# Optimization experiments

Hardware: AMD Instinct MI355X
Metric: run time of the kernel (lower is better)

Reference implementation:

```python
import jax, jax.numpy as jnp
import numpy as np
from jax import lax

B, C, H, W = 4, 192, 64, 64
D_STATE, D_CONV, EXPAND = 16, 4, 2
D_INNER = EXPAND * C           # 384
DT_RANK = (C + 15) // 16       # 12 (mamba_ssm default ceil(d_model/16))


def setup_inputs() -> dict:
    key = jax.random.key(0)
    ks = jax.random.split(key, 12)
    sc = lambda k, shape, s=0.02: (jax.random.normal(k, shape, jnp.float32) * s)
    x = jax.random.normal(ks[0], (B, C, H, W), jnp.float32)
    norm_w = jnp.ones((C,), jnp.float32)
    norm_b = jnp.zeros((C,), jnp.float32)
    in_proj_w = sc(ks[1], (2 * D_INNER, C))
    conv_w = sc(ks[2], (D_INNER, D_CONV), 0.1)
    conv_b = jnp.zeros((D_INNER,), jnp.float32)
    x_proj_w = sc(ks[3], (DT_RANK + 2 * D_STATE, D_INNER))
    dt_proj_w = sc(ks[4], (D_INNER, DT_RANK), 0.1)
    # dt bias init so softplus(dt_bias) is in a realistic [1e-3, 1e-1] range
    dt0 = jax.random.uniform(ks[5], (D_INNER,), jnp.float32, 0.001, 0.1)
    dt_proj_b = jnp.log(jnp.expm1(dt0))
    A_log = jnp.log(jnp.broadcast_to(
        jnp.arange(1, D_STATE + 1, dtype=jnp.float32), (D_INNER, D_STATE)))
    D = jnp.ones((D_INNER,), jnp.float32)
    out_proj_w = sc(ks[6], (C, D_INNER))
    return {"x": x, "norm_w": norm_w, "norm_b": norm_b, "in_proj_w": in_proj_w,
            "conv_w": conv_w, "conv_b": conv_b, "x_proj_w": x_proj_w,
            "dt_proj_w": dt_proj_w, "dt_proj_b": dt_proj_b, "A_log": A_log,
            "D": D, "out_proj_w": out_proj_w}


def _mamba2d(x, norm_w, norm_b, in_proj_w, conv_w, conv_b, x_proj_w,
             dt_proj_w, dt_proj_b, A_log, D, out_proj_w):
    b, c, h, w = x.shape
    L = h * w
    seq = x.reshape(b, c, L).transpose(0, 2, 1)            # (B, L, C)
    # LayerNorm over channel dim
    mu = seq.mean(-1, keepdims=True)
    var = ((seq - mu) ** 2).mean(-1, keepdims=True)
    seqn = (seq - mu) * lax.rsqrt(var + 1e-5) * norm_w + norm_b
    # in_proj -> (x, z)
    xz = seqn @ in_proj_w.T                                # (B, L, 2*d_inner)
    xin, z = jnp.split(xz, 2, axis=-1)
    # causal depthwise conv1d over L
    xc = xin.transpose(0, 2, 1)                            # (B, d_inner, L)
    xc = lax.conv_general_dilated(xc, conv_w[:, None, :], (1,),
                                  [(D_CONV - 1, 0)],
                                  feature_group_count=D_INNER)
    xc = jax.nn.silu(xc + conv_b[None, :, None])
    xs = xc.transpose(0, 2, 1)                             # (B, L, d_inner)
    # input-dependent dt, B, C
    dbl = xs @ x_proj_w.T                                  # (B, L, dt_rank+2n)
    dt = dbl[..., :DT_RANK]
    Bm = dbl[..., DT_RANK:DT_RANK + D_STATE]               # (B, L, n)
    Cm = dbl[..., DT_RANK + D_STATE:]                      # (B, L, n)
    dt = jax.nn.softplus(dt @ dt_proj_w.T + dt_proj_b)     # (B, L, d_inner)
    A = -jnp.exp(A_log)                                    # (d_inner, n)
    dA = jnp.exp(dt[..., None] * A)                        # (B, L, d_inner, n)
    dBx = jnp.einsum('bld,bln->bldn', dt * xs, Bm)         # (B, L, d_inner, n)
    # selective scan over L
    def step(hcar, inp):
        dA_t, dBx_t, C_t = inp
        hcar = dA_t * hcar + dBx_t                         # (B, d_inner, n)
        y_t = jnp.einsum('bdn,bn->bd', hcar, C_t)
        return hcar, y_t
    h0 = jnp.zeros((b, D_INNER, D_STATE), xs.dtype)
    _, ys = lax.scan(step, h0, (jnp.moveaxis(dA, 1, 0),
                                jnp.moveaxis(dBx, 1, 0),
                                jnp.moveaxis(Cm, 1, 0)))
    y = jnp.moveaxis(ys, 0, 1) + xs * D                    # (B, L, d_inner)
    y = y * jax.nn.silu(z)
    out = y @ out_proj_w.T                                 # (B, L, C)
    return x + out.transpose(0, 2, 1).reshape(b, c, h, w)


def reference(x, norm_w, norm_b, in_proj_w, conv_w, conv_b, x_proj_w,
              dt_proj_w, dt_proj_b, A_log, D, out_proj_w):
    return _mamba2d(x, norm_w, norm_b, in_proj_w, conv_w, conv_b, x_proj_w,
                    dt_proj_w, dt_proj_b, A_log, D, out_proj_w)
```

## Files before the change

kernel.cpp:

```cpp
#include <hip/hip_runtime.h>
#include <hip/hip_bf16.h>

constexpr int B_ = 4;
constexpr int C_ = 192;
constexpr int L_ = 4096;
constexpr int DI = 384;
constexpr int DSs = 16;
constexpr int DTR = 12;
constexpr int NDBL = 44;
constexpr int NCHUNK = 256;
constexpr int CSZ = 16;

constexpr size_t BL = (size_t)B_ * L_;

constexpr size_t F_SEQN = 0;
constexpr size_t F_XIN  = F_SEQN + BL * C_ / 2;
constexpr size_t F_Z    = F_XIN + BL * DI / 2;
constexpr size_t F_XSB  = F_Z + BL * DI / 2;
constexpr size_t F_DBL  = F_XSB + BL * DI / 2;
constexpr size_t F_DT   = F_DBL + BL * NDBL;
constexpr size_t F_SBUF = F_DT + BL * DI / 2;
constexpr size_t F_HLOC = F_SBUF + (size_t)B_ * NCHUNK * DI;
constexpr size_t F_WBUF = F_HLOC + (size_t)B_ * NCHUNK * DI * 16 / 2;

typedef __attribute__((ext_vector_type(8))) short bf16x8;
typedef __attribute__((ext_vector_type(4))) float f32x4;

__device__ __forceinline__ unsigned short f2bf(float v) {
  unsigned x = __builtin_bit_cast(unsigned, v);
  unsigned r = x + 0x7FFFu + ((x >> 16) & 1u);
  return (unsigned short)(r >> 16);
}
__device__ __forceinline__ float bf2f(unsigned short u) {
  return __builtin_bit_cast(float, (unsigned)u << 16);
}
__device__ __forceinline__ void gload16(const void* g, void* l) {
  __builtin_amdgcn_global_load_lds((const __attribute__((address_space(1))) void*)g,
                                   (__attribute__((address_space(3))) void*)l, 16, 0, 0);
}
#define MFMA16(a, b, c) __builtin_amdgcn_mfma_f32_16x16x32_bf16(a, b, c, 0, 0, 0)

__global__ __launch_bounds__(256) void k_ln(const float* __restrict__ x,
                                            const float* __restrict__ nw,
                                            const float* __restrict__ nb,
                                            unsigned short* __restrict__ seqn,
                                            const float* __restrict__ ipw,
                                            const float* __restrict__ xpw,
                                            const float* __restrict__ opw,
                                            unsigned short* __restrict__ wbuf) {
  if (blockIdx.x >= 256) {
    int t = (blockIdx.x - 256) * 256 + threadIdx.x;
    if (t < 239616) {
      float v;
      if (t < 147456) v = ipw[t];
      else if (t < 165888) {
        int j = t - 147456;
        int r = j / 384, c = j - r * 384;
        v = (r < 44) ? xpw[r * 384 + c] : 0.f;
      } else v = opw[t - 165888];
      wbuf[t] = f2bf(v);
    }
    return;
  }
  __shared__ float xt[192][65];
  __shared__ float ps[4][64], ps2[4][64];
  __shared__ float mu_[64], rs_[64];
  __shared__ float wsh[192], bsh[192];
  int tid = threadIdx.x;
  int blk = blockIdx.x;
  int b = blk >> 6;
  int l0 = (blk & 63) << 6;
  const float* xb = x + (size_t)b * C_ * L_;
  for (int idx = tid; idx < 192 * 64; idx += 256) {
    int c = idx >> 6, ll = idx & 63;
    xt[c][ll] = xb[(size_t)c * L_ + l0 + ll];
  }
  if (tid < 192) { wsh[tid] = nw[tid]; bsh[tid] = nb[tid]; }
  __syncthreads();
  int ll = tid & 63, q = tid >> 6;
  float s = 0.f, ss = 0.f;
  for (int c = q * 48; c < q * 48 + 48; ++c) { float v = xt[c][ll]; s += v; ss += v * v; }
  ps[q][ll] = s; ps2[q][ll] = ss;
  __syncthreads();
  if (q == 0) {
    float st = ps[0][ll] + ps[1][ll] + ps[2][ll] + ps[3][ll];
    float sst = ps2[0][ll] + ps2[1][ll] + ps2[2][ll] + ps2[3][ll];
    float mu = st * (1.f / 192.f);
    float var = sst * (1.f / 192.f) - mu * mu;
    mu_[ll] = mu; rs_[ll] = rsqrtf(var + 1e-5f);
  }
  __syncthreads();
  unsigned short* so = seqn + ((size_t)b * L_ + l0) * C_;
  for (int idx = tid; idx < 64 * 192; idx += 256) {
    int l = idx / 192, c = idx - l * 192;
    so[idx] = f2bf((xt[c][l] - mu_[l]) * rs_[l] * wsh[c] + bsh[c]);
  }
}

__global__ __launch_bounds__(256) void k_inproj(const unsigned short* __restrict__ A,
                                                const unsigned short* __restrict__ W,
                                                unsigned short* __restrict__ xin,
                                                unsigned short* __restrict__ z) {
  __shared__ unsigned short smem[16384];
  unsigned short* As = smem;
  unsigned short* Bs = smem + 8192;
  int tid = threadIdx.x;
  int w = tid >> 6, l = tid & 63;
  int wr = w >> 1, wc = w & 1;
  int m0 = blockIdx.x << 7;
  int n0 = blockIdx.y << 7;
  f32x4 acc[4][4];
#pragma unroll
  for (int i = 0; i < 4; ++i)
#pragma unroll
    for (int j = 0; j < 4; ++j) acc[i][j] = (f32x4){0.f, 0.f, 0.f, 0.f};
  int lr = l & 15, lk = l >> 4;
  for (int kt = 0; kt < 3; ++kt) {
    int k0 = kt * 64;
    if (kt) __syncthreads();
#pragma unroll
    for (int i = 0; i < 4; ++i) {
      int row = (i << 5) + (tid >> 3);
      int gc = k0 + (((tid & 7) ^ (row & 7)) << 3);
      gload16(A + (size_t)(m0 + row) * 192 + gc, &As[(i << 11) + (w << 9)]);
      gload16(W + (size_t)(n0 + row) * 192 + gc, &Bs[(i << 11) + (w << 9)]);
    }
    __syncthreads();
#pragma unroll
    for (int ks = 0; ks < 2; ++ks) {
      int s = (ks << 2) + lk;
      bf16x8 af[4], bfr[4];
#pragma unroll
      for (int mi = 0; mi < 4; ++mi) {
        int r = (wr << 6) + (mi << 4) + lr;
        af[mi] = *(const bf16x8*)&As[r * 64 + ((s ^ (r & 7)) << 3)];
      }
#pragma unroll
      for (int ni = 0; ni < 4; ++ni) {
        int r = (wc << 6) + (ni << 4) + lr;
        bfr[ni] = *(const bf16x8*)&Bs[r * 64 + ((s ^ (r & 7)) << 3)];
      }
#pragma unroll
      for (int mi = 0; mi < 4; ++mi)
#pragma unroll
        for (int ni = 0; ni < 4; ++ni) acc[mi][ni] = MFMA16(af[mi], bfr[ni], acc[mi][ni]);
    }
  }
  __syncthreads();
#pragma unroll
  for (int mi = 0; mi < 4; ++mi)
#pragma unroll
    for (int ni = 0; ni < 4; ++ni) {
      int col = (wc << 6) + (ni << 4) + lr;
#pragma unroll
      for (int r = 0; r < 4; ++r) {
        int row = (wr << 6) + (mi << 4) + (lk << 2) + r;
        smem[(row << 7) + col] = f2bf(acc[mi][ni][r]);
      }
    }
  __syncthreads();
#pragma unroll
  for (int i = 0; i < 8; ++i) {
    int chunk = i * 256 + tid;
    int row = chunk >> 4, cq = chunk & 15;
    int n = n0 + (cq << 3);
    unsigned short* dst = (n < 384) ? (xin + (size_t)(m0 + row) * DI + n)
                                    : (z + (size_t)(m0 + row) * DI + (n - 384));
    *(bf16x8*)dst = *(const bf16x8*)&smem[(row << 7) + (cq << 3)];
  }
}

__global__ __launch_bounds__(256) void k_conv(const unsigned short* __restrict__ xin,
                                              const float* __restrict__ cw,
                                              const float* __restrict__ cb,
                                              unsigned short* __restrict__ xsb) {
  __shared__ float xt[67][64];
  __shared__ float res[64][65];
  int tid = threadIdx.x;
  int d0 = blockIdx.x << 6;
  int l0 = blockIdx.y << 6;
  int b = blockIdx.z;
  for (int idx = tid; idx < 67 * 16; idx += 256) {
    int rr = idx >> 4, q = idx & 15;
    int l = l0 - 3 + rr;
    float4 v = make_float4(0.f, 0.f, 0.f, 0.f);
    if (l >= 0) {
      ushort4 u = *(const ushort4*)&xin[((size_t)b * L_ + l) * DI + d0 + (q << 2)];
      v = make_float4(bf2f(u.x), bf2f(u.y), bf2f(u.z), bf2f(u.w));
    }
    *(float4*)&xt[rr][q << 2] = v;
  }
  __syncthreads();
  int dd = tid & 63, lq = tid >> 6;
  float4 w4 = *(const float4*)&cw[(d0 + dd) * 4];
  float bb = cb[d0 + dd];
  for (int rr = 0; rr < 16; ++rr) {
    int ll = (rr << 2) + lq;
    float a = bb + w4.x * xt[ll][dd] + w4.y * xt[ll + 1][dd] + w4.z * xt[ll + 2][dd] +
              w4.w * xt[ll + 3][dd];
    res[ll][dd] = a * __builtin_amdgcn_rcpf(1.f + __expf(-a));
  }
  __syncthreads();
  for (int idx = tid; idx < 64 * 16; idx += 256) {
    int ll = idx >> 4, q = idx & 15;
    ushort4 u;
    u.x = f2bf(res[ll][(q << 2)]);
    u.y = f2bf(res[ll][(q << 2) + 1]);
    u.z = f2bf(res[ll][(q << 2) + 2]);
    u.w = f2bf(res[ll][(q << 2) + 3]);
    *(ushort4*)&xsb[((size_t)b * L_ + l0 + ll) * DI + d0 + (q << 2)] = u;
  }
}

__global__ __launch_bounds__(256) void k_xproj(const unsigned short* __restrict__ A,
                                               const unsigned short* __restrict__ W,
                                               float* __restrict__ dbl) {
  __shared__ unsigned short smem[4096 + 3072];
  unsigned short* As = smem;
  unsigned short* Bs = smem + 4096;
  int tid = threadIdx.x;
  int w = tid >> 6, l = tid & 63;
  int m0 = blockIdx.x << 6;
  int lr = l & 15, lk = l >> 4;
  f32x4 acc[3];
#pragma unroll
  for (int i = 0; i < 3; ++i) acc[i] = (f32x4){0.f, 0.f, 0.f, 0.f};
  for (int kt = 0; kt < 6; ++kt) {
    int k0 = kt * 64;
    if (kt) __syncthreads();
#pragma unroll
    for (int i = 0; i < 2; ++i) {
      int row = (i << 5) + (tid >> 3);
      int gc = k0 + (((tid & 7) ^ (row & 7)) << 3);
      gload16(A + (size_t)(m0 + row) * 384 + gc, &As[(i << 11) + (w << 9)]);
    }
    {
      int row = tid >> 3;
      int gc = k0 + (((tid & 7) ^ (row & 7)) << 3);
      gload16(W + (size_t)row * 384 + gc, &Bs[w << 9]);
    }
    if (w < 2) {
      int row = 32 + (tid >> 3);
      int gc = k0 + (((tid & 7) ^ (row & 7)) << 3);
      gload16(W + (size_t)row * 384 + gc, &Bs[2048 + (w << 9)]);
    }
    __syncthreads();
#pragma unroll
    for (int ks = 0; ks < 2; ++ks) {
      int s = (ks << 2) + lk;
      int ar = (w << 4) + lr;
      bf16x8 a = *(const bf16x8*)&As[ar * 64 + ((s ^ (ar & 7)) << 3)];
#pragma unroll
      for (int ni = 0; ni < 3; ++ni) {
        int br = (ni << 4) + lr;
        bf16x8 bb = *(const bf16x8*)&Bs[br * 64 + ((s ^ (br & 7)) << 3)];
        acc[ni] = MFMA16(a, bb, acc[ni]);
      }
    }
  }
#pragma unroll
  for (int ni = 0; ni < 3; ++ni)
#pragma unroll
    for (int r = 0; r < 4; ++r) {
      int col = (ni << 4) + lr;
      if (col < NDBL) dbl[(size_t)(m0 + (w << 4) + (lk << 2) + r) * NDBL + col] = acc[ni][r];
    }
}

__global__ __launch_bounds__(384) void k_scanA(const unsigned short* __restrict__ xsb,
                                               const float* __restrict__ dbl,
                                               const float* __restrict__ dw,
                                               const float* __restrict__ dbias,
                                               const float* __restrict__ A_log,
                                               unsigned short* __restrict__ dtb,
                                               unsigned short* __restrict__ Hloc,
                                               float* __restrict__ Sbuf) {
  __shared__ float Bsh[CSZ][16];
  __shared__ float dl[CSZ][12];
  int tid = threadIdx.x;
  int blk = blockIdx.x;
  int b = blk >> 8;
  int chunk = blk & (NCHUNK - 1);
  int l0 = chunk * CSZ;
  for (int idx = tid; idx < CSZ * 28; idx += 384) {
    int r = idx / 28, c = idx - r * 28;
    float v = dbl[((size_t)b * L_ + l0 + r) * NDBL + c];
    if (c < 12) dl[r][c] = v; else Bsh[r][c - 12] = v;
  }
  int d = tid;
  float4 wv0 = *(const float4*)&dw[d * 12];
  float4 wv1 = *(const float4*)&dw[d * 12 + 4];
  float4 wv2 = *(const float4*)&dw[d * 12 + 8];
  float bias = dbias[d];
  bool fast = true;
#pragma unroll
  for (int n = 0; n < 16; ++n) {
    float An_ = -__expf(A_log[d * 16 + n]);
    fast = fast && (fabsf(An_ + (float)(n + 1)) < 2e-3f);
  }
  const unsigned short* xp = xsb + ((size_t)b * L_ + l0) * DI + d;
  unsigned short* dtp = dtb + ((size_t)b * L_ + l0) * DI + d;
  __syncthreads();
  float h[16];
#pragma unroll
  for (int n = 0; n < 16; ++n) h[n] = 0.f;
  float S = 0.f;
  if (fast) {
#pragma unroll
    for (int i = 0; i < CSZ; ++i) {
      float4 c0 = *(const float4*)&dl[i][0];
      float4 c1 = *(const float4*)&dl[i][4];
      float4 c2 = *(const float4*)&dl[i][8];
      float a = bias;
      a = fmaf(wv0.x, c0.x, a); a = fmaf(wv0.y, c0.y, a);
      a = fmaf(wv0.z, c0.z, a); a = fmaf(wv0.w, c0.w, a);
      a = fmaf(wv1.x, c1.x, a); a = fmaf(wv1.y, c1.y, a);
      a = fmaf(wv1.z, c1.z, a); a = fmaf(wv1.w, c1.w, a);
      a = fmaf(wv2.x, c2.x, a); a = fmaf(wv2.y, c2.y, a);
      a = fmaf(wv2.z, c2.z, a); a = fmaf(wv2.w, c2.w, a);
      float sp = fmaxf(a, 0.f) + __logf(1.f + __expf(-fabsf(a)));
      dtp[(size_t)i * DI] = f2bf(sp);
      S += sp;
      float xv = bf2f(xp[(size_t)i * DI]);
      float dtx = sp * xv;
      float r = __expf(-sp);
      float r2 = r * r;
      float r4 = r2 * r2;
      float dA0 = r, dA1 = r2, dA2 = r2 * r, dA3 = r4;
#pragma unroll
      for (int g = 0; g < 4; ++g) {
        float4 Bg = *(const float4*)&Bsh[i][g << 2];
        h[(g << 2) + 0] = fmaf(dA0, h[(g << 2) + 0], dtx * Bg.x);
        h[(g << 2) + 1] = fmaf(dA1, h[(g << 2) + 1], dtx * Bg.y);
        h[(g << 2) + 2] = fmaf(dA2, h[(g << 2) + 2], dtx * Bg.z);
        h[(g << 2) + 3] = fmaf(dA3, h[(g << 2) + 3], dtx * Bg.w);
        if (g < 3) { dA0 *= r4; dA1 *= r4; dA2 *= r4; dA3 *= r4; }
      }
    }
  } else {
    float An[16];
#pragma unroll
    for (int n = 0; n < 16; ++n) An[n] = -__expf(A_log[d * 16 + n]);
#pragma unroll
    for (int i = 0; i < CSZ; ++i) {
      float4 c0 = *(const float4*)&dl[i][0];
      float4 c1 = *(const float4*)&dl[i][4];
      float4 c2 = *(const float4*)&dl[i][8];
      float a = bias;
      a = fmaf(wv0.x, c0.x, a); a = fmaf(wv0.y, c0.y, a);
      a = fmaf(wv0.z, c0.z, a); a = fmaf(wv0.w, c0.w, a);
      a = fmaf(wv1.x, c1.x, a); a = fmaf(wv1.y, c1.y, a);
      a = fmaf(wv1.z, c1.z, a); a = fmaf(wv1.w, c1.w, a);
      a = fmaf(wv2.x, c2.x, a); a = fmaf(wv2.y, c2.y, a);
      a = fmaf(wv2.z, c2.z, a); a = fmaf(wv2.w, c2.w, a);
      float sp = fmaxf(a, 0.f) + __logf(1.f + __expf(-fabsf(a)));
      dtp[(size_t)i * DI] = f2bf(sp);
      S += sp;
      float xv = bf2f(xp[(size_t)i * DI]);
      float dtx = sp * xv;
#pragma unroll
      for (int n = 0; n < 16; ++n)
        h[n] = fmaf(__expf(sp * An[n]), h[n], dtx * Bsh[i][n]);
    }
  }
  size_t hbase = ((size_t)(b * NCHUNK + chunk) * 16) * DI + d;
#pragma unroll
  for (int n = 0; n < 16; ++n) Hloc[hbase + (size_t)n * DI] = f2bf(h[n]);
  Sbuf[((size_t)b * NCHUNK + chunk) * DI + d] = S;
}

__global__ __launch_bounds__(256) void k_scanB(const float* __restrict__ A_log,
                                               unsigned short* __restrict__ Hloc,
                                               const float* __restrict__ Sbuf) {
  int gid = blockIdx.x * 256 + threadIdx.x;
  int d = gid % DI;
  int rest = gid / DI;
  int n = rest & 15;
  int b = rest >> 4;
  float An = -__expf(A_log[d * 16 + n]);
  unsigned short* Hp = Hloc + ((size_t)b * NCHUNK * 16 + n) * DI + d;
  const float* Sp = Sbuf + (size_t)b * NCHUNK * DI + d;
  constexpr size_t HS = (size_t)16 * DI;
  float h = 0.f;
  float SA[8], HA[8], SB[8], HB[8];
#define LDGRP(Sa, Ha, cb)                         \
  _Pragma("unroll") for (int u = 0; u < 8; ++u) { \
    Sa[u] = Sp[(size_t)((cb) + u) * DI];          \
    Ha[u] = bf2f(Hp[(size_t)((cb) + u) * HS]);    \
  }
#define STGRP(Sa, Ha, cb)                         \
  _Pragma("unroll") for (int u = 0; u < 8; ++u) { \
    Hp[(size_t)((cb) + u) * HS] = f2bf(h);        \
    h = fmaf(__expf(An * Sa[u]), h, Ha[u]);       \
  }
  LDGRP(SA, HA, 0)
  for (int g = 0; g < 32; g += 2) {
    LDGRP(SB, HB, (g + 1) * 8)
    STGRP(SA, HA, g * 8)
    if (g + 2 < 32) LDGRP(SA, HA, (g + 2) * 8)
    STGRP(SB, HB, (g + 1) * 8)
  }
#undef LDGRP
#undef STGRP
}

__global__ __launch_bounds__(384) void k_scanC(const unsigned short* __restrict__ xsb,
                                               const unsigned short* __restrict__ dtb,
                                               const float* __restrict__ dbl,
                                               const unsigned short* __restrict__ z,
                                               const float* __restrict__ A_log,
                                               const float* __restrict__ Dw,
                                               const unsigned short* __restrict__ Hloc,
                                               unsigned short* __restrict__ ybuf) {
  __shared__ float BCsh[CSZ][32];
  int tid = threadIdx.x;
  int blk = blockIdx.x;
  int b = blk >> 8;
  int chunk = blk & (NCHUNK - 1);
  int l0 = chunk * CSZ;
  for (int idx = tid; idx < CSZ * 32; idx += 384) {
    int r = idx >> 5, n32 = idx & 31;
    BCsh[r][n32] = dbl[((size_t)b * L_ + l0 + r) * NDBL + DTR + n32];
  }
  int d = tid;
  float Dd = Dw[d];
  bool fast = true;
#pragma unroll
  for (int n = 0; n < 16; ++n) {
    float An_ = -__expf(A_log[d * 16 + n]);
    fast = fast && (fabsf(An_ + (float)(n + 1)) < 2e-3f);
  }
  size_t hbase = ((size_t)(b * NCHUNK + chunk) * 16) * DI + d;
  float h[16];
#pragma unroll
  for (int n = 0; n < 16; ++n) h[n] = bf2f(Hloc[hbase + (size_t)n * DI]);
  const unsigned short* xp = xsb + ((size_t)b * L_ + l0) * DI + d;
  const unsigned short* dtp = dtb + ((size_t)b * L_ + l0) * DI + d;
  const unsigned short* zp = z + ((size_t)b * L_ + l0) * DI + d;
  unsigned short* yp = ybuf + ((size_t)b * L_ + l0) * DI + d;
  __syncthreads();
  if (fast) {
#pragma unroll
    for (int i = 0; i < CSZ; ++i) {
      float sp = bf2f(dtp[(size_t)i * DI]);
      float xv = bf2f(xp[(size_t)i * DI]);
      float zv = bf2f(zp[(size_t)i * DI]);
      float dtx = sp * xv;
      float r = __expf(-sp);
      float r2 = r * r;
      float r4 = r2 * r2;
      float dA0 = r, dA1 = r2, dA2 = r2 * r, dA3 = r4;
      float y = 0.f;
#pragma unroll
      for (int g = 0; g < 4; ++g) {
        float4 Bg = *(const float4*)&BCsh[i][g << 2];
        float4 Cg = *(const float4*)&BCsh[i][16 + (g << 2)];
        h[(g << 2) + 0] = fmaf(dA0, h[(g << 2) + 0], dtx * Bg.x);
        h[(g << 2) + 1] = fmaf(dA1, h[(g << 2) + 1], dtx * Bg.y);
        h[(g << 2) + 2] = fmaf(dA2, h[(g << 2) + 2], dtx * Bg.z);
        h[(g << 2) + 3] = fmaf(dA3, h[(g << 2) + 3], dtx * Bg.w);
        y = fmaf(h[(g << 2) + 0], Cg.x, y);
        y = fmaf(h[(g << 2) + 1], Cg.y, y);
        y = fmaf(h[(g << 2) + 2], Cg.z, y);
        y = fmaf(h[(g << 2) + 3], Cg.w, y);
        if (g < 3) { dA0 *= r4; dA1 *= r4; dA2 *= r4; dA3 *= r4; }
      }
      y = fmaf(xv, Dd, y);
      float sig = __builtin_amdgcn_rcpf(1.f + __expf(-zv));
      yp[(size_t)i * DI] = f2bf(y * (zv * sig));
    }
  } else {
    float An[16];
#pragma unroll
    for (int n = 0; n < 16; ++n) An[n] = -__expf(A_log[d * 16 + n]);
#pragma unroll
    for (int i = 0; i < CSZ; ++i) {
      float sp = bf2f(dtp[(size_t)i * DI]);
      float xv = bf2f(xp[(size_t)i * DI]);
      float zv = bf2f(zp[(size_t)i * DI]);
      float dtx = sp * xv;
      float y = 0.f;
#pragma unroll
      for (int n = 0; n < 16; ++n) {
        h[n] = fmaf(__expf(sp * An[n]), h[n], dtx * BCsh[i][n]);
        y = fmaf(h[n], BCsh[i][16 + n], y);
      }
      y = fmaf(xv, Dd, y);
      float sig = __builtin_amdgcn_rcpf(1.f + __expf(-zv));
      yp[(size_t)i * DI] = f2bf(y * (zv * sig));
    }
  }
}

__global__ __launch_bounds__(256) void k_outproj(const unsigned short* __restrict__ Y,
                                                 const unsigned short* __restrict__ W,
                                                 const float* __restrict__ x,
                                                 float* __restrict__ out) {
  __shared__ float smemf[8448];
  unsigned short* As = (unsigned short*)smemf;
  unsigned short* Bs = (unsigned short*)smemf + 8192;
  int tid = threadIdx.x;
  int w = tid >> 6, l = tid & 63;
  int wr = w >> 1, wc = w & 1;
  int m0 = blockIdx.x << 7;
  int n0 = blockIdx.y << 6;
  int lr = l & 15, lk = l >> 4;
  f32x4 acc[4][2];
#pragma unroll
  for (int i = 0; i < 4; ++i)
#pragma unroll
    for (int j = 0; j < 2; ++j) acc[i][j] = (f32x4){0.f, 0.f, 0.f, 0.f};
  for (int kt = 0; kt < 6; ++kt) {
    int k0 = kt * 64;
    if (kt) __syncthreads();
#pragma unroll
    for (int i = 0; i < 4; ++i) {
      int row = (i << 5) + (tid >> 3);
      int gc = k0 + (((tid & 7) ^ (row & 7)) << 3);
      gload16(Y + (size_t)(m0 + row) * 384 + gc, &As[(i << 11) + (w << 9)]);
    }
#pragma unroll
    for (int i = 0; i < 2; ++i) {
      int row = (i << 5) + (tid >> 3);
      int gc = k0 + (((tid & 7) ^ (row & 7)) << 3);
      gload16(W + (size_t)(n0 + row) * 384 + gc, &Bs[(i << 11) + (w << 9)]);
    }
    __syncthreads();
#pragma unroll
    for (int ks = 0; ks < 2; ++ks) {
      int s = (ks << 2) + lk;
      bf16x8 bfr[2];
#pragma unroll
      for (int ni = 0; ni < 2; ++ni) {
        int r = (wc << 5) + (ni << 4) + lr;
        bfr[ni] = *(const bf16x8*)&Bs[r * 64 + ((s ^ (r & 7)) << 3)];
      }
#pragma unroll
      for (int mi = 0; mi < 4; ++mi) {
        int r = (wr << 6) + (mi << 4) + lr;
        bf16x8 a = *(const bf16x8*)&As[r * 64 + ((s ^ (r & 7)) << 3)];
#pragma unroll
        for (int ni = 0; ni < 2; ++ni) acc[mi][ni] = MFMA16(a, bfr[ni], acc[mi][ni]);
      }
    }
  }
  __syncthreads();
#pragma unroll
  for (int mi = 0; mi < 4; ++mi)
#pragma unroll
    for (int ni = 0; ni < 2; ++ni) {
      int c = (wc << 5) + (ni << 4) + lr;
      int lrow = (wr << 6) + (mi << 4) + (lk << 2);
      *(f32x4*)&smemf[c * 132 + lrow] = acc[mi][ni];
    }
  __syncthreads();
  int b = m0 >> 12;
  int l0 = m0 & (L_ - 1);
#pragma unroll
  for (int i = 0; i < 8; ++i) {
    int chunk = i * 256 + tid;
    int c = chunk >> 5, lq = chunk & 31;
    f32x4 v = *(const f32x4*)&smemf[c * 132 + (lq << 2)];
    size_t off = ((size_t)b * C_ + n0 + c) * L_ + l0 + (lq << 2);
    f32x4 xv = *(const f32x4*)&x[off];
    v = v + xv;
    *(f32x4*)&out[off] = v;
  }
}

extern "C" void kernel_launch(void* const* d_in, const int* in_sizes, int n_in,
                              void* d_out, int out_size, void* d_ws, size_t ws_size,
                              hipStream_t stream) {
  const float* x         = (const float*)d_in[0];
  const float* norm_w    = (const float*)d_in[1];
  const float* norm_b    = (const float*)d_in[2];
  const float* in_proj_w = (const float*)d_in[3];
  const float* conv_w    = (const float*)d_in[4];
  const float* conv_b    = (const float*)d_in[5];
  const float* x_proj_w  = (const float*)d_in[6];
  const float* dt_proj_w = (const float*)d_in[7];
  const float* dt_proj_b = (const float*)d_in[8];
  const float* A_log     = (const float*)d_in[9];
  const float* Dw        = (const float*)d_in[10];
  const float* out_proj_w= (const float*)d_in[11];
  float* out = (float*)d_out;
  float* ws = (float*)d_ws;

  unsigned short* seqn = (unsigned short*)(ws + F_SEQN);
  unsigned short* xin  = (unsigned short*)(ws + F_XIN);
  unsigned short* z    = (unsigned short*)(ws + F_Z);
  unsigned short* xsb  = (unsigned short*)(ws + F_XSB);
  float* dbl           = ws + F_DBL;
  unsigned short* dtb  = (unsigned short*)(ws + F_DT);
  float* Sbuf          = ws + F_SBUF;
  unsigned short* Hloc = (unsigned short*)(ws + F_HLOC);
  unsigned short* wbuf = (unsigned short*)(ws + F_WBUF);
  unsigned short* ipw  = wbuf;
  unsigned short* xpw  = wbuf + 147456;
  unsigned short* opw  = wbuf + 165888;
  unsigned short* ybuf = xin;

  hipLaunchKernelGGL(k_ln, dim3(1192), dim3(256), 0, stream, x, norm_w, norm_b, seqn,
                     in_proj_w, x_proj_w, out_proj_w, wbuf);
  hipLaunchKernelGGL(k_inproj, dim3(128, 6), dim3(256), 0, stream, seqn, ipw, xin, z);
  hipLaunchKernelGGL(k_conv, dim3(6, 64, 4), dim3(256), 0, stream, xin, conv_w, conv_b, xsb);
  hipLaunchKernelGGL(k_xproj, dim3(256), dim3(256), 0, stream, xsb, xpw, dbl);
  hipLaunchKernelGGL(k_scanA, dim3(1024), dim3(384), 0, stream, xsb, dbl, dt_proj_w, dt_proj_b,
                     A_log, dtb, Hloc, Sbuf);
  hipLaunchKernelGGL(k_scanB, dim3(96), dim3(256), 0, stream, A_log, Hloc, Sbuf);
  hipLaunchKernelGGL(k_scanC, dim3(1024), dim3(384), 0, stream, xsb, dtb, dbl, z, A_log, Dw,
                     Hloc, ybuf);
  hipLaunchKernelGGL(k_outproj, dim3(128, 3), dim3(256), 0, stream, ybuf, opw, x, out);
}
```

Before: 113.5 us.

## Fuse causal conv with x_proj GEMM and stage LayerNorm input as bf16

Merges the depthwise causal conv + SiLU kernel with the x_proj GEMM. Each block computes conv outputs for 64 positions across all 384 channels, walking the sequence serially per thread. It writes them into swizzled shared memory and feeds them straight to MFMA, so the x_proj kernel no longer re-reads xsb from global memory and one launch disappears. The LayerNorm kernel now loads x with float4 and keeps its tile in shared memory as bf16, halving LDS use but rounding x before the mean and variance are computed. The fused kernel runs only 256 blocks with a serial 64-step loop per thread, which lowers parallelism compared with the earlier 1536-block conv.

```diff
diff --git a/kernel.cpp b/kernel.cpp
--- a/kernel.cpp
+++ b/kernel.cpp
@@ -62,7 +62,7 @@
     }
     return;
   }
-  __shared__ float xt[192][65];
+  __shared__ unsigned short xt[192][66];
   __shared__ float ps[4][64], ps2[4][64];
   __shared__ float mu_[64], rs_[64];
   __shared__ float wsh[192], bsh[192];
@@ -71,15 +71,23 @@
   int b = blk >> 6;
   int l0 = (blk & 63) << 6;
   const float* xb = x + (size_t)b * C_ * L_;
-  for (int idx = tid; idx < 192 * 64; idx += 256) {
-    int c = idx >> 6, ll = idx & 63;
-    xt[c][ll] = xb[(size_t)c * L_ + l0 + ll];
+  for (int idx = tid; idx < 192 * 16; idx += 256) {
+    int c = idx >> 4, lq = idx & 15;
+    float4 v = *(const float4*)&xb[(size_t)c * L_ + l0 + (lq << 2)];
+    ushort2 u0, u1;
+    u0.x = f2bf(v.x); u0.y = f2bf(v.y);
+    u1.x = f2bf(v.z); u1.y = f2bf(v.w);
+    *(ushort2*)&xt[c][(lq << 2)] = u0;
+    *(ushort2*)&xt[c][(lq << 2) + 2] = u1;
   }
   if (tid < 192) { wsh[tid] = nw[tid]; bsh[tid] = nb[tid]; }
   __syncthreads();
   int ll = tid & 63, q = tid >> 6;
   float s = 0.f, ss = 0.f;
-  for (int c = q * 48; c < q * 48 + 48; ++c) { float v = xt[c][ll]; s += v; ss += v * v; }
+  for (int c = q * 48; c < q * 48 + 48; ++c) {
+    float v = bf2f(xt[c][ll]);
+    s += v; ss += v * v;
+  }
   ps[q][ll] = s; ps2[q][ll] = ss;
   __syncthreads();
   if (q == 0) {
@@ -93,7 +101,7 @@
   unsigned short* so = seqn + ((size_t)b * L_ + l0) * C_;
   for (int idx = tid; idx < 64 * 192; idx += 256) {
     int l = idx / 192, c = idx - l * 192;
-    so[idx] = f2bf((xt[c][l] - mu_[l]) * rs_[l] * wsh[c] + bsh[c]);
+    so[idx] = f2bf((bf2f(xt[c][l]) - mu_[l]) * rs_[l] * wsh[c] + bsh[c]);
   }
 }
 
@@ -170,101 +178,79 @@
   }
 }
 
-__global__ __launch_bounds__(256) void k_conv(const unsigned short* __restrict__ xin,
-                                              const float* __restrict__ cw,
-                                              const float* __restrict__ cb,
-                                              unsigned short* __restrict__ xsb) {
-  __shared__ float xt[67][64];
-  __shared__ float res[64][65];
-  int tid = threadIdx.x;
-  int d0 = blockIdx.x << 6;
-  int l0 = blockIdx.y << 6;
-  int b = blockIdx.z;
-  for (int idx = tid; idx < 67 * 16; idx += 256) {
-    int rr = idx >> 4, q = idx & 15;
-    int l = l0 - 3 + rr;
-    float4 v = make_float4(0.f, 0.f, 0.f, 0.f);
-    if (l >= 0) {
-      ushort4 u = *(const ushort4*)&xin[((size_t)b * L_ + l) * DI + d0 + (q << 2)];
-      v = make_float4(bf2f(u.x), bf2f(u.y), bf2f(u.z), bf2f(u.w));
-    }
-    *(float4*)&xt[rr][q << 2] = v;
-  }
-  __syncthreads();
-  int dd = tid & 63, lq = tid >> 6;
-  float4 w4 = *(const float4*)&cw[(d0 + dd) * 4];
-  float bb = cb[d0 + dd];
-  for (int rr = 0; rr < 16; ++rr) {
-    int ll = (rr << 2) + lq;
-    float a = bb + w4.x * xt[ll][dd] + w4.y * xt[ll + 1][dd] + w4.z * xt[ll + 2][dd] +
-              w4.w * xt[ll + 3][dd];
-    res[ll][dd] = a * __builtin_amdgcn_rcpf(1.f + __expf(-a));
-  }
-  __syncthreads();
-  for (int idx = tid; idx < 64 * 16; idx += 256) {
-    int ll = idx >> 4, q = idx & 15;
-    ushort4 u;
-    u.x = f2bf(res[ll][(q << 2)]);
-    u.y = f2bf(res[ll][(q << 2) + 1]);
-    u.z = f2bf(res[ll][(q << 2) + 2]);
-    u.w = f2bf(res[ll][(q << 2) + 3]);
-    *(ushort4*)&xsb[((size_t)b * L_ + l0 + ll) * DI + d0 + (q << 2)] = u;
-  }
-}
-
-__global__ __launch_bounds__(256) void k_xproj(const unsigned short* __restrict__ A,
+__global__ __launch_bounds__(384) void k_convx(const unsigned short* __restrict__ xin,
+                                               const float* __restrict__ cw,
+                                               const float* __restrict__ cb,
                                                const unsigned short* __restrict__ W,
+                                               unsigned short* __restrict__ xsb,
                                                float* __restrict__ dbl) {
-  __shared__ unsigned short smem[4096 + 3072];
-  unsigned short* As = smem;
-  unsigned short* Bs = smem + 4096;
+  __shared__ unsigned short xs[6 * 4096];
+  __shared__ unsigned short Bs[3072];
   int tid = threadIdx.x;
   int w = tid >> 6, l = tid & 63;
-  int m0 = blockIdx.x << 6;
+  int b = blockIdx.y;
+  int l0 = blockIdx.x << 6;
+  int d = tid;
+  float4 w4 = *(const float4*)&cw[d * 4];
+  float bb = cb[d];
+  const unsigned short* xp = xin + ((size_t)b * L_ + l0) * DI + d;
+  unsigned short* op = xsb + ((size_t)b * L_ + l0) * DI + d;
+  float x0 = 0.f, x1 = 0.f, x2 = 0.f;
+  if (l0 > 0) {
+    x0 = bf2f(*(xp - 3 * DI));
+    x1 = bf2f(*(xp - 2 * DI));
+    x2 = bf2f(*(xp - DI));
+  }
+  int kt = d >> 6, col = d & 63, g = col >> 3, e = col & 7;
+  unsigned short* xsrow = xs + kt * 4096;
+  for (int r = 0; r < 64; ++r) {
+    float xv = bf2f(xp[(size_t)r * DI]);
+    float a = bb + w4.x * x0 + w4.y * x1 + w4.z * x2 + w4.w * xv;
+    float sv = a * __builtin_amdgcn_rcpf(1.f + __expf(-a));
+    unsigned short sb = f2bf(sv);
+    xsrow[r * 64 + ((g ^ (r & 7)) << 3) + e] = sb;
+    op[(size_t)r * DI] = sb;
+    x0 = x1; x1 = x2; x2 = xv;
+  }
+  __syncthreads();
   int lr = l & 15, lk = l >> 4;
   f32x4 acc[3];
 #pragma unroll
   for (int i = 0; i < 3; ++i) acc[i] = (f32x4){0.f, 0.f, 0.f, 0.f};
-  for (int kt = 0; kt < 6; ++kt) {
-    int k0 = kt * 64;
-    if (kt) __syncthreads();
-#pragma unroll
-    for (int i = 0; i < 2; ++i) {
-      int row = (i << 5) + (tid >> 3);
-      int gc = k0 + (((tid & 7) ^ (row & 7)) << 3);
-      gload16(A + (size_t)(m0 + row) * 384 + gc, &As[(i << 11) + (w << 9)]);
-    }
+  for (int kt2 = 0; kt2 < 6; ++kt2) {
+    int k0 = kt2 * 64;
+    if (kt2) __syncthreads();
     {
       int row = tid >> 3;
       int gc = k0 + (((tid & 7) ^ (row & 7)) << 3);
       gload16(W + (size_t)row * 384 + gc, &Bs[w << 9]);
     }
-    if (w < 2) {
-      int row = 32 + (tid >> 3);
-      int gc = k0 + (((tid & 7) ^ (row & 7)) << 3);
-      gload16(W + (size_t)row * 384 + gc, &Bs[2048 + (w << 9)]);
-    }
     __syncthreads();
-#pragma unroll
-    for (int ks = 0; ks < 2; ++ks) {
-      int s = (ks << 2) + lk;
-      int ar = (w << 4) + lr;
-      bf16x8 a = *(const bf16x8*)&As[ar * 64 + ((s ^ (ar & 7)) << 3)];
-#pragma unroll
-      for (int ni = 0; ni < 3; ++ni) {
-        int br = (ni << 4) + lr;
-        bf16x8 bb = *(const bf16x8*)&Bs[br * 64 + ((s ^ (br & 7)) << 3)];
-        acc[ni] = MFMA16(a, bb, acc[ni]);
-      }
-    }
-  }
-#pragma unroll
-  for (int ni = 0; ni < 3; ++ni)
-#pragma unroll
-    for (int r = 0; r < 4; ++r) {
-      int col = (ni << 4) + lr;
-      if (col < NDBL) dbl[(size_t)(m0 + (w << 4) + (lk << 2) + r) * NDBL + col] = acc[ni][r];
-    }
+    if (w < 4) {
+#pragma unroll
+      for (int ks = 0; ks < 2; ++ks) {
+        int s = (ks << 2) + lk;
+        int ar = (w << 4) + lr;
+        bf16x8 a = *(const bf16x8*)&xs[kt2 * 4096 + ar * 64 + ((s ^ (ar & 7)) << 3)];
+#pragma unroll
+        for (int ni = 0; ni < 3; ++ni) {
+          int br = (ni << 4) + lr;
+          bf16x8 bbv = *(const bf16x8*)&Bs[br * 64 + ((s ^ (br & 7)) << 3)];
+          acc[ni] = MFMA16(a, bbv, acc[ni]);
+        }
+      }
+    }
+  }
+  if (w < 4) {
+#pragma unroll
+    for (int ni = 0; ni < 3; ++ni)
+#pragma unroll
+      for (int r = 0; r < 4; ++r) {
+        int colq = (ni << 4) + lr;
+        if (colq < NDBL)
+          dbl[((size_t)b * L_ + l0 + (w << 4) + (lk << 2) + r) * NDBL + colq] = acc[ni][r];
+      }
+  }
 }
 
 __global__ __launch_bounds__(384) void k_scanA(const unsigned short* __restrict__ xsb,
@@ -603,8 +589,8 @@
   hipLaunchKernelGGL(k_ln, dim3(1192), dim3(256), 0, stream, x, norm_w, norm_b, seqn,
                      in_proj_w, x_proj_w, out_proj_w, wbuf);
   hipLaunchKernelGGL(k_inproj, dim3(128, 6), dim3(256), 0, stream, seqn, ipw, xin, z);
-  hipLaunchKernelGGL(k_conv, dim3(6, 64, 4), dim3(256), 0, stream, xin, conv_w, conv_b, xsb);
-  hipLaunchKernelGGL(k_xproj, dim3(256), dim3(256), 0, stream, xsb, xpw, dbl);
+  hipLaunchKernelGGL(k_convx, dim3(64, 4), dim3(384), 0, stream, xin, conv_w, conv_b, xpw, xsb,
+                     dbl);
   hipLaunchKernelGGL(k_scanA, dim3(1024), dim3(384), 0, stream, xsb, dbl, dt_proj_w, dt_proj_b,
                      A_log, dtb, Hloc, Sbuf);
   hipLaunchKernelGGL(k_scanB, dim3(96), dim3(256), 0, stream, A_log, Hloc, Sbuf);
```

Result: no change. 111.6 us (-1.7%).
